# Kernel optimization log

Hardware: AMD Instinct MI355X
Metric: run time of the kernel (lower is better)

The kernel has to match this reference:

```python
import jax, jax.numpy as jnp
import numpy as np

IN_DIM = 128
LAYER_DIMS = [128, 128]
NUM_SAMPLES = [25, 10]
L0 = 3072
NEG_WEIGHT = 1.0


def setup_inputs() -> dict:
    key = jax.random.key(0)
    ks = jax.random.split(key, 12)
    feat = jax.random.normal(ks[0], (L0, IN_DIM), dtype=jnp.float32)
    nodes = jax.random.randint(ks[1], (L0,), 0, L0)
    nb0 = jnp.arange(L0)
    nb1 = jax.random.randint(ks[2], (L0 * 10,), 0, L0)
    nb2 = jax.random.randint(ks[3], (L0 * 10 * 25,), 0, L0)
    src_idx = jax.random.randint(ks[4], (1024,), 0, L0)
    pos_idx = jax.random.randint(ks[5], (1024,), 0, L0)
    neg_idx = jax.random.randint(ks[6], (512,), 0, L0)
    g = 0.05
    # mean aggregator weights: layer0 in=IN_DIM, layer1 in=2*128 (concat)
    w_self_0 = jax.random.normal(ks[7], (IN_DIM, 128), jnp.float32) * g
    w_neigh_0 = jax.random.normal(ks[8], (IN_DIM, 128), jnp.float32) * g
    w_self_1 = jax.random.normal(ks[9], (256, 128), jnp.float32) * g
    w_neigh_1 = jax.random.normal(ks[10], (256, 128), jnp.float32) * g
    return dict(nodes=nodes, feat=feat, src_idx=src_idx, pos_idx=pos_idx,
                neg_idx=neg_idx, nb0=nb0, nb1=nb1, nb2=nb2,
                w_self_0=w_self_0, w_neigh_0=w_neigh_0,
                w_self_1=w_self_1, w_neigh_1=w_neigh_1)


def _aggregate(hidden, params):
    # GraphSAGE layer stack: at layer l, combine each hop with the mean of its
    # sampled neighbors, concat self/neigh transforms, relu except last layer.
    num_layers = len(NUM_SAMPLES)
    for layer in range(num_layers):
        w_self, w_neigh = params[layer]
        is_last = layer == num_layers - 1
        next_hidden = []
        for hop in range(num_layers - layer):
            s = NUM_SAMPLES[num_layers - hop - 1]
            self_v = hidden[hop]  # [n, d]
            neigh = hidden[hop + 1].reshape(self_v.shape[0], s, self_v.shape[1])
            neigh_mean = jnp.mean(neigh, axis=1)
            h = jnp.concatenate([self_v @ w_self, neigh_mean @ w_neigh], axis=1)
            if not is_last:
                h = jax.nn.relu(h)
            next_hidden.append(h)
        hidden = next_hidden
    return hidden[0]


def _l2_normalize(x, eps=1e-12):
    return x * jax.lax.rsqrt(jnp.maximum(jnp.sum(x * x, axis=1, keepdims=True), eps))


def reference(nodes, feat, src_idx, pos_idx, neg_idx, nb0, nb1, nb2,
              w_self_0, w_neigh_0, w_self_1, w_neigh_1):
    hidden = [feat[nb0], feat[nb1], feat[nb2]]
    params = [(w_self_0, w_neigh_0), (w_self_1, w_neigh_1)]
    output = _aggregate(hidden, params)          # [L0, 256]
    output = _l2_normalize(output)
    src_emb = output[src_idx]                    # [B, 256]
    pos_emb = output[pos_idx]
    neg_emb = output[neg_idx]                    # [Nneg, 256]

    aff = jnp.sum(src_emb * pos_emb, axis=1)     # [B]
    neg_aff = src_emb @ neg_emb.T                # [B, Nneg]

    # MRR via double argsort (tf double top_k equivalent; ties -> positive last)
    aff_all = jnp.concatenate([neg_aff, aff[:, None]], axis=1)
    order = jnp.argsort(-aff_all, axis=1, stable=True)
    ranks = jnp.argsort(order, axis=1, stable=True)
    mrr = jnp.mean(1.0 / (ranks[:, -1].astype(jnp.float32) + 1.0))

    # sigmoid cross-entropy: labels 1 -> softplus(-x); labels 0 -> softplus(x)
    true_xent = jax.nn.softplus(-aff)
    neg_xent = jax.nn.softplus(neg_aff)
    loss = jnp.sum(true_xent) + NEG_WEIGHT * jnp.sum(neg_xent)
    loss = loss / jnp.asarray(src_emb.shape[0], jnp.float32)
    return src_emb, loss, mrr
```

## Files before the change

### kernel.cpp

```cpp
#include <hip/hip_runtime.h>
#include <math.h>

#define L0      3072
#define BATCH   1024
#define NNEG    512


__device__ __forceinline__ float bf2f(unsigned short u) {
  return __uint_as_float(((unsigned)u) << 16);
}
__device__ __forceinline__ void store_out(float v, float* p) { *p = v; }
__device__ __forceinline__ void store_out(float v, unsigned short* p) {
  unsigned x = __float_as_uint(v);
  *p = (unsigned short)((x + 0x7fff + ((x >> 16) & 1)) >> 16);
}

template<int K, int AW, int HOFF, bool NORM, typename OutT>
__global__ __launch_bounds__(512) void k_mm(
    const float* __restrict__ Ain,
    const float* __restrict__ W0, const float* __restrict__ W1,
    OutT* __restrict__ Out, const int ldo, const int outHalfOff,
    float* __restrict__ zbuf, const int zcount) {
  __shared__ float AT[6 * AW];
  __shared__ float rs[8][3];
  const int t = threadIdx.x;
  if (zbuf != nullptr && blockIdx.x == 0)
    for (int z = t; z < zcount; z += 512) zbuf[z] = 0.f;
  const int base = blockIdx.x * 6;
  {
    const float4* __restrict__ src = (const float4*)(Ain + base * AW);
    float4* __restrict__ dst = (float4*)AT;
    for (int idx = t; idx < 6 * AW / 4; idx += 512) dst[idx] = src[idx];
  }
  __syncthreads();

  const int wave = t >> 6;
  const int half = wave >> 2;
  const int colg = (wave >> 1) & 1;
  const int rowg = wave & 1;
  const int rg = rowg * 3;
  const int col = colg * 64 + (t & 63);
  const float* __restrict__ W = (half ? W1 : W0) + col;
  const float* __restrict__ A0 = AT + rg * AW + half * HOFF;

  float acc[3] = {0.f, 0.f, 0.f};
#pragma unroll 4
  for (int d = 0; d < K; d += 4) {
    float4 a[3];
#pragma unroll
    for (int r = 0; r < 3; ++r) a[r] = *(const float4*)&A0[r * AW + d];
    float w[4];
#pragma unroll
    for (int i2 = 0; i2 < 4; ++i2) w[i2] = W[(d + i2) * 128];
#pragma unroll
    for (int i2 = 0; i2 < 4; ++i2)
#pragma unroll
      for (int r = 0; r < 3; ++r)
        acc[r] = fmaf(((const float*)&a[r])[i2], w[i2], acc[r]);
  }

  float scale[3] = {1.f, 1.f, 1.f};
  if (NORM) {
    float p[3];
#pragma unroll
    for (int r = 0; r < 3; ++r) p[r] = acc[r] * acc[r];
#pragma unroll
    for (int off = 32; off > 0; off >>= 1)
#pragma unroll
      for (int r = 0; r < 3; ++r) p[r] += __shfl_xor(p[r], off, 64);
    if ((t & 63) == 0) { rs[wave][0] = p[0]; rs[wave][1] = p[1]; rs[wave][2] = p[2]; }
    __syncthreads();
#pragma unroll
    for (int r = 0; r < 3; ++r) {
      const float s = rs[rowg][r] + rs[rowg + 2][r] + rs[rowg + 4][r] + rs[rowg + 6][r];
      scale[r] = rsqrtf(fmaxf(s, 1e-12f));
    }
  }
  OutT* __restrict__ O = Out + half * outHalfOff;
#pragma unroll
  for (int r = 0; r < 3; ++r)
    store_out(acc[r] * scale[r], &O[(base + rg + r) * ldo + col]);
}

__global__ __launch_bounds__(640) void k_aggregate(
    const unsigned short* __restrict__ X0, const unsigned short* __restrict__ Y0,
    const int* __restrict__ nb0, const int* __restrict__ nb1,
    const int* __restrict__ nb2, float* __restrict__ H) {
  __shared__ float gB[10][128], gC[10][128], gD[10][128];
  const int i = blockIdx.x;
  const int t = threadIdx.x;
  const int n0 = nb0[i];
  const int j = t >> 6;
  const int lam = t & 63;
  const int r = i * 10 + j;
  int myidx = 0;
  if (lam < 25) myidx = nb2[r * 25 + lam];
  else if (lam == 25) myidx = nb1[r];
  const int c8 = lam & 15;
  const int sub = lam >> 4;

  float d8[8];
#pragma unroll
  for (int e = 0; e < 8; ++e) d8[e] = 0.f;
#pragma unroll
  for (int m = 0; m < 7; ++m) {
    const int k = sub + 4 * m;
    const int ridx = __shfl(myidx, k, 64);
    if (k < 25) {
      const float4 raw = *(const float4*)(Y0 + ridx * 128 + c8 * 8);
      const unsigned short* u = (const unsigned short*)&raw;
#pragma unroll
      for (int e = 0; e < 8; ++e) d8[e] += bf2f(u[e]);
    }
  }
#pragma unroll
  for (int e = 0; e < 8; ++e) d8[e] += __shfl_xor(d8[e], 16, 64);
#pragma unroll
  for (int e = 0; e < 8; ++e) d8[e] += __shfl_xor(d8[e], 32, 64);

  const int r1 = __shfl(myidx, 25, 64);
  if (sub == 0) {
#pragma unroll
    for (int e = 0; e < 8; ++e) gD[j][c8 * 8 + e] = fmaxf(d8[e] * 0.04f, 0.f);
    const float4 raw = *(const float4*)(Y0 + r1 * 128 + c8 * 8);
    const unsigned short* u = (const unsigned short*)&raw;
#pragma unroll
    for (int e = 0; e < 8; ++e) gB[j][c8 * 8 + e] = bf2f(u[e]);
  } else if (sub == 1) {
    const float4 raw = *(const float4*)(X0 + r1 * 128 + c8 * 8);
    const unsigned short* u = (const unsigned short*)&raw;
#pragma unroll
    for (int e = 0; e < 8; ++e) gC[j][c8 * 8 + e] = fmaxf(bf2f(u[e]), 0.f);
  }
  __syncthreads();

  if (t < 512) {
    const int q = t >> 7, c = t & 127;
    float v;
    if (q == 0) {
      v = fmaxf(bf2f(X0[n0 * 128 + c]), 0.f);
    } else {
      const float* g = (q == 1) ? &gB[0][0] : (q == 2) ? &gC[0][0] : &gD[0][0];
      float s = 0.f;
#pragma unroll
      for (int jj = 0; jj < 10; ++jj) s += g[jj * 128 + c];
      v = s * 0.1f;
      if (q == 1) v = fmaxf(v, 0.f);
    }
    H[i * 512 + t] = v;
  }
}

__device__ __forceinline__ float softplusf(float x) {
  return fmaxf(x, 0.f) + log1pf(expf(-fabsf(x)));
}

__global__ __launch_bounds__(256) void k_prep(
    const float* __restrict__ R, const int* __restrict__ neg_idx,
    float* __restrict__ NT) {
  const int idx = blockIdx.x * 256 + threadIdx.x;
  const int c = idx & 511;
  const int d4 = idx >> 9;
  const float4 v = *(const float4*)&R[neg_idx[c] * 256 + d4 * 4];
#pragma unroll
  for (int i2 = 0; i2 < 4; ++i2)
    NT[(d4 * 4 + i2) * 512 + c] = ((const float*)&v)[i2];
}

__global__ __launch_bounds__(256) void k_neg(
    const float* __restrict__ O, const float* __restrict__ NT,
    const int* __restrict__ src_idx, const int* __restrict__ pos_idx,
    float* __restrict__ out_src, int* __restrict__ rank,
    float* __restrict__ spPos, float* __restrict__ spNeg,
    int* __restrict__ done) {
  __shared__ float SP[32 * 260];
  __shared__ float affL[16];
  __shared__ int cntL[16];
  __shared__ float wsum[4];
  __shared__ int lastDone;
  const int t = threadIdx.x;
  const int rowBase = (blockIdx.x >> 2) * 16;
  const int colBase = (blockIdx.x & 3) * 128;
  const bool first = (colBase == 0);

  if (t < 16) cntL[t] = 0;

  {
    const float4* __restrict__ s4 = (const float4*)O;
#pragma unroll
    for (int idx = t; idx < 32 * 64; idx += 256) {
      const int row = idx >> 6, c4 = idx & 63;
      const int rid = (row < 16) ? src_idx[rowBase + row]
                                 : pos_idx[rowBase + row - 16];
      *(float4*)&SP[row * 260 + c4 * 4] = s4[rid * 64 + c4];
    }
  }
  if (first) {
    const float4* __restrict__ s4 = (const float4*)O;
    float4* __restrict__ d4o = (float4*)out_src;
#pragma unroll
    for (int idx = t; idx < 16 * 64; idx += 256) {
      const int rr = idx >> 6, c4 = idx & 63;
      d4o[(rowBase + rr) * 64 + c4] = s4[src_idx[rowBase + rr] * 64 + c4];
    }
  }
  __syncthreads();

  const int tc = t & 31;
  const int tr = t >> 5;
  const float* __restrict__ B = NT + colBase + 4 * tc;
  const float* __restrict__ A0 = SP + tr * 260;
  const float* __restrict__ A1 = SP + (tr + 8) * 260;
  const float* __restrict__ SV = SP + t * 260;
  const float* __restrict__ PV = SP + (16 + t) * 260;

  float acc[2][4];
#pragma unroll
  for (int r = 0; r < 2; ++r)
#pragma unroll
    for (int j = 0; j < 4; ++j) acc[r][j] = 0.f;
  float aff = 0.f;

#pragma unroll 2
  for (int d4 = 0; d4 < 64; ++d4) {
    const int dd = d4 * 4;
    const float4 a0 = *(const float4*)&A0[dd];
    const float4 a1 = *(const float4*)&A1[dd];
    float4 b[4];
#pragma unroll
    for (int i2 = 0; i2 < 4; ++i2)
      b[i2] = *(const float4*)&B[(dd + i2) * 512];
    float4 sv, pv;
    if (t < 16) {
      sv = *(const float4*)&SV[dd];
      pv = *(const float4*)&PV[dd];
    }
#pragma unroll
    for (int i2 = 0; i2 < 4; ++i2) {
      const float va0 = ((const float*)&a0)[i2];
      const float va1 = ((const float*)&a1)[i2];
#pragma unroll
      for (int j = 0; j < 4; ++j) {
        const float vb = ((const float*)&b[i2])[j];
        acc[0][j] = fmaf(va0, vb, acc[0][j]);
        acc[1][j] = fmaf(va1, vb, acc[1][j]);
      }
      if (t < 16)
        aff = fmaf(((const float*)&sv)[i2], ((const float*)&pv)[i2], aff);
    }
  }
  if (t < 16) affL[t] = aff;
  __syncthreads();

  float sp = 0.f;
  int cnt[2] = {0, 0};
#pragma unroll
  for (int r = 0; r < 2; ++r) {
    const float av = affL[tr + 8 * r];
#pragma unroll
    for (int j = 0; j < 4; ++j) {
      const float v = acc[r][j];
      sp += softplusf(v);
      cnt[r] += (v >= av) ? 1 : 0;
    }
  }
  if (cnt[0]) atomicAdd(&cntL[tr], cnt[0]);
  if (cnt[1]) atomicAdd(&cntL[tr + 8], cnt[1]);
#pragma unroll
  for (int off = 32; off > 0; off >>= 1) sp += __shfl_down(sp, off, 64);
  if ((t & 63) == 0) wsum[t >> 6] = sp;
  if (first && t < 16) atomicAdd(spPos, softplusf(-aff));
  __syncthreads();
  if (t == 0) atomicAdd(spNeg, wsum[0] + wsum[1] + wsum[2] + wsum[3]);
  if (t < 16) atomicAdd(&rank[rowBase + t], cntL[t]);

  __threadfence();
  __syncthreads();
  if (t == 0) lastDone = (atomicAdd(done, 1) == 255) ? 1 : 0;
  __syncthreads();
  if (lastDone) {
    float s = 0.f;
    for (int i = t; i < BATCH; i += 256) {
      const int rv = __hip_atomic_load(&rank[i], __ATOMIC_RELAXED,
                                       __HIP_MEMORY_SCOPE_AGENT);
      s += 1.f / (float)(rv + 1);
    }
#pragma unroll
    for (int off = 32; off > 0; off >>= 1) s += __shfl_down(s, off, 64);
    if ((t & 63) == 0) wsum[t >> 6] = s;
    __syncthreads();
    if (t == 0) {
      const float mrr = (wsum[0] + wsum[1] + wsum[2] + wsum[3]) * (1.f / 1024.f);
      const float p = __hip_atomic_load(spPos, __ATOMIC_RELAXED,
                                        __HIP_MEMORY_SCOPE_AGENT);
      const float n = __hip_atomic_load(spNeg, __ATOMIC_RELAXED,
                                        __HIP_MEMORY_SCOPE_AGENT);
      out_src[BATCH * 256]     = (p + n) * (1.f / 1024.f);
      out_src[BATCH * 256 + 1] = mrr;
    }
  }
}

extern "C" void kernel_launch(void* const* d_in, const int* in_sizes, int n_in,
                              void* d_out, int out_size, void* d_ws, size_t ws_size,
                              hipStream_t stream) {
  const float* feat   = (const float*)d_in[1];
  const int* src_idx  = (const int*)d_in[2];
  const int* pos_idx  = (const int*)d_in[3];
  const int* neg_idx  = (const int*)d_in[4];
  const int* nb0      = (const int*)d_in[5];
  const int* nb1      = (const int*)d_in[6];
  const int* nb2      = (const int*)d_in[7];
  const float* ws0    = (const float*)d_in[8];
  const float* wn0    = (const float*)d_in[9];
  const float* ws1    = (const float*)d_in[10];
  const float* wn1    = (const float*)d_in[11];

  float* wsf = (float*)d_ws;
  unsigned short* X0 = (unsigned short*)d_ws;
  unsigned short* Y0 = X0 + 393216;
  float* H     = wsf + 393216;
  float* R     = wsf + 1966080;
  float* spPos = wsf + 2752512;
  float* spNeg = wsf + 2752513;
  int*   rank  = (int*)(wsf + 2752514);
  int*   done  = rank + 1024;
  float* NT    = wsf + 2753540;
  float* out   = (float*)d_out;

  k_mm<128, 128, 0, false, unsigned short><<<L0 / 6, 512, 0, stream>>>(
      feat, ws0, wn0, X0, 128, 393216, spPos, 1027);
  k_aggregate<<<L0, 640, 0, stream>>>(X0, Y0, nb0, nb1, nb2, H);
  k_mm<256, 512, 256, true, float><<<L0 / 6, 512, 0, stream>>>(
      H, ws1, wn1, R, 256, 128, nullptr, 0);
  k_prep<<<128, 256, 0, stream>>>(R, neg_idx, NT);
  k_neg<<<256, 256, 0, stream>>>(
      R, NT, src_idx, pos_idx, out, rank, spPos, spNeg, done);
}
```

Before: 166.6 us.

## Fuse all stages into one persistent kernel with software grid barriers

Replaces the five launches (two GEMMs, aggregation, transpose prep, negative scoring) with a zeroing kernel plus one 256-block persistent kernel that uses atomic-counter grid barriers between phases. The aggregation now keeps its per-node hidden rows in shared memory and feeds the second GEMM directly, which removes the H round trip through global memory. The intent is to cut launch gaps and intermediate traffic. In exchange the whole pipeline runs on only 256 blocks, so parallelism in the gather and GEMM phases is much lower. The spin barriers also depend on all blocks being resident at once.

```diff
diff --git a/kernel.cpp b/kernel.cpp
--- a/kernel.cpp
+++ b/kernel.cpp
@@ -4,299 +4,362 @@
 #define L0      3072
 #define BATCH   1024
 #define NNEG    512
+#define NBLK    256
 
 
 __device__ __forceinline__ float bf2f(unsigned short u) {
   return __uint_as_float(((unsigned)u) << 16);
 }
-__device__ __forceinline__ void store_out(float v, float* p) { *p = v; }
-__device__ __forceinline__ void store_out(float v, unsigned short* p) {
+__device__ __forceinline__ unsigned short f2bf(float v) {
   unsigned x = __float_as_uint(v);
-  *p = (unsigned short)((x + 0x7fff + ((x >> 16) & 1)) >> 16);
-}
-
-template<int K, int AW, int HOFF, bool NORM, typename OutT>
-__global__ __launch_bounds__(512) void k_mm(
-    const float* __restrict__ Ain,
-    const float* __restrict__ W0, const float* __restrict__ W1,
-    OutT* __restrict__ Out, const int ldo, const int outHalfOff,
-    float* __restrict__ zbuf, const int zcount) {
-  __shared__ float AT[6 * AW];
-  __shared__ float rs[8][3];
-  const int t = threadIdx.x;
-  if (zbuf != nullptr && blockIdx.x == 0)
-    for (int z = t; z < zcount; z += 512) zbuf[z] = 0.f;
-  const int base = blockIdx.x * 6;
-  {
-    const float4* __restrict__ src = (const float4*)(Ain + base * AW);
-    float4* __restrict__ dst = (float4*)AT;
-    for (int idx = t; idx < 6 * AW / 4; idx += 512) dst[idx] = src[idx];
-  }
-  __syncthreads();
-
-  const int wave = t >> 6;
-  const int half = wave >> 2;
-  const int colg = (wave >> 1) & 1;
-  const int rowg = wave & 1;
-  const int rg = rowg * 3;
-  const int col = colg * 64 + (t & 63);
-  const float* __restrict__ W = (half ? W1 : W0) + col;
-  const float* __restrict__ A0 = AT + rg * AW + half * HOFF;
-
-  float acc[3] = {0.f, 0.f, 0.f};
-#pragma unroll 4
-  for (int d = 0; d < K; d += 4) {
-    float4 a[3];
-#pragma unroll
-    for (int r = 0; r < 3; ++r) a[r] = *(const float4*)&A0[r * AW + d];
-    float w[4];
-#pragma unroll
-    for (int i2 = 0; i2 < 4; ++i2) w[i2] = W[(d + i2) * 128];
-#pragma unroll
-    for (int i2 = 0; i2 < 4; ++i2)
-#pragma unroll
-      for (int r = 0; r < 3; ++r)
-        acc[r] = fmaf(((const float*)&a[r])[i2], w[i2], acc[r]);
-  }
-
-  float scale[3] = {1.f, 1.f, 1.f};
-  if (NORM) {
-    float p[3];
-#pragma unroll
-    for (int r = 0; r < 3; ++r) p[r] = acc[r] * acc[r];
-#pragma unroll
-    for (int off = 32; off > 0; off >>= 1)
-#pragma unroll
-      for (int r = 0; r < 3; ++r) p[r] += __shfl_xor(p[r], off, 64);
-    if ((t & 63) == 0) { rs[wave][0] = p[0]; rs[wave][1] = p[1]; rs[wave][2] = p[2]; }
-    __syncthreads();
-#pragma unroll
-    for (int r = 0; r < 3; ++r) {
-      const float s = rs[rowg][r] + rs[rowg + 2][r] + rs[rowg + 4][r] + rs[rowg + 6][r];
-      scale[r] = rsqrtf(fmaxf(s, 1e-12f));
-    }
-  }
-  OutT* __restrict__ O = Out + half * outHalfOff;
-#pragma unroll
-  for (int r = 0; r < 3; ++r)
-    store_out(acc[r] * scale[r], &O[(base + rg + r) * ldo + col]);
-}
-
-__global__ __launch_bounds__(640) void k_aggregate(
-    const unsigned short* __restrict__ X0, const unsigned short* __restrict__ Y0,
-    const int* __restrict__ nb0, const int* __restrict__ nb1,
-    const int* __restrict__ nb2, float* __restrict__ H) {
-  __shared__ float gB[10][128], gC[10][128], gD[10][128];
-  const int i = blockIdx.x;
-  const int t = threadIdx.x;
-  const int n0 = nb0[i];
-  const int j = t >> 6;
-  const int lam = t & 63;
-  const int r = i * 10 + j;
-  int myidx = 0;
-  if (lam < 25) myidx = nb2[r * 25 + lam];
-  else if (lam == 25) myidx = nb1[r];
-  const int c8 = lam & 15;
-  const int sub = lam >> 4;
-
-  float d8[8];
-#pragma unroll
-  for (int e = 0; e < 8; ++e) d8[e] = 0.f;
-#pragma unroll
-  for (int m = 0; m < 7; ++m) {
-    const int k = sub + 4 * m;
-    const int ridx = __shfl(myidx, k, 64);
-    if (k < 25) {
-      const float4 raw = *(const float4*)(Y0 + ridx * 128 + c8 * 8);
-      const unsigned short* u = (const unsigned short*)&raw;
-#pragma unroll
-      for (int e = 0; e < 8; ++e) d8[e] += bf2f(u[e]);
-    }
-  }
-#pragma unroll
-  for (int e = 0; e < 8; ++e) d8[e] += __shfl_xor(d8[e], 16, 64);
-#pragma unroll
-  for (int e = 0; e < 8; ++e) d8[e] += __shfl_xor(d8[e], 32, 64);
-
-  const int r1 = __shfl(myidx, 25, 64);
-  if (sub == 0) {
-#pragma unroll
-    for (int e = 0; e < 8; ++e) gD[j][c8 * 8 + e] = fmaxf(d8[e] * 0.04f, 0.f);
-    const float4 raw = *(const float4*)(Y0 + r1 * 128 + c8 * 8);
-    const unsigned short* u = (const unsigned short*)&raw;
-#pragma unroll
-    for (int e = 0; e < 8; ++e) gB[j][c8 * 8 + e] = bf2f(u[e]);
-  } else if (sub == 1) {
-    const float4 raw = *(const float4*)(X0 + r1 * 128 + c8 * 8);
-    const unsigned short* u = (const unsigned short*)&raw;
-#pragma unroll
-    for (int e = 0; e < 8; ++e) gC[j][c8 * 8 + e] = fmaxf(bf2f(u[e]), 0.f);
-  }
-  __syncthreads();
-
-  if (t < 512) {
-    const int q = t >> 7, c = t & 127;
-    float v;
-    if (q == 0) {
-      v = fmaxf(bf2f(X0[n0 * 128 + c]), 0.f);
-    } else {
-      const float* g = (q == 1) ? &gB[0][0] : (q == 2) ? &gC[0][0] : &gD[0][0];
-      float s = 0.f;
-#pragma unroll
-      for (int jj = 0; jj < 10; ++jj) s += g[jj * 128 + c];
-      v = s * 0.1f;
-      if (q == 1) v = fmaxf(v, 0.f);
-    }
-    H[i * 512 + t] = v;
-  }
-}
-
+  return (unsigned short)((x + 0x7fff + ((x >> 16) & 1)) >> 16);
+}
 __device__ __forceinline__ float softplusf(float x) {
   return fmaxf(x, 0.f) + log1pf(expf(-fabsf(x)));
 }
 
-__global__ __launch_bounds__(256) void k_prep(
-    const float* __restrict__ R, const int* __restrict__ neg_idx,
-    float* __restrict__ NT) {
-  const int idx = blockIdx.x * 256 + threadIdx.x;
-  const int c = idx & 511;
-  const int d4 = idx >> 9;
-  const float4 v = *(const float4*)&R[neg_idx[c] * 256 + d4 * 4];
-#pragma unroll
-  for (int i2 = 0; i2 < 4; ++i2)
-    NT[(d4 * 4 + i2) * 512 + c] = ((const float*)&v)[i2];
-}
-
-__global__ __launch_bounds__(256) void k_neg(
-    const float* __restrict__ O, const float* __restrict__ NT,
-    const int* __restrict__ src_idx, const int* __restrict__ pos_idx,
-    float* __restrict__ out_src, int* __restrict__ rank,
+__device__ __forceinline__ void gbar(int* ctr) {
+  __syncthreads();
+  if (threadIdx.x == 0) {
+    __threadfence();
+    __hip_atomic_fetch_add(ctr, 1, __ATOMIC_ACQ_REL, __HIP_MEMORY_SCOPE_AGENT);
+    while (__hip_atomic_load(ctr, __ATOMIC_ACQUIRE,
+                             __HIP_MEMORY_SCOPE_AGENT) < NBLK)
+      __builtin_amdgcn_s_sleep(1);
+  }
+  __syncthreads();
+}
+
+struct D2S {
+  float SP[32 * 260];
+  float affL[16];
+  int   cntL[16];
+  float wsum[8];
+  int   lastDone;
+};
+union SMU {
+  float AT[12 * 512];
+  D2S   d2;
+};
+
+__global__ __launch_bounds__(256) void k_zero(float* z) {
+  const int t = threadIdx.x;
+  for (int i = t; i < 1030; i += 256) z[i] = 0.f;
+}
+
+__global__ __launch_bounds__(512) void k_fused(
+    const float* __restrict__ feat, const int* __restrict__ src_idx,
+    const int* __restrict__ pos_idx, const int* __restrict__ neg_idx,
+    const int* __restrict__ nb0, const int* __restrict__ nb1,
+    const int* __restrict__ nb2,
+    const float* __restrict__ ws0, const float* __restrict__ wn0,
+    const float* __restrict__ ws1, const float* __restrict__ wn1,
+    unsigned short* __restrict__ X0, unsigned short* __restrict__ Y0,
+    float* __restrict__ R, float* __restrict__ NT,
     float* __restrict__ spPos, float* __restrict__ spNeg,
-    int* __restrict__ done) {
-  __shared__ float SP[32 * 260];
-  __shared__ float affL[16];
-  __shared__ int cntL[16];
-  __shared__ float wsum[4];
-  __shared__ int lastDone;
+    int* __restrict__ rank, int* __restrict__ done, int* __restrict__ bar,
+    float* __restrict__ out) {
+  __shared__ SMU sm;
+  __shared__ float rs2[8][3];
   const int t = threadIdx.x;
-  const int rowBase = (blockIdx.x >> 2) * 16;
-  const int colBase = (blockIdx.x & 3) * 128;
-  const bool first = (colBase == 0);
-
-  if (t < 16) cntL[t] = 0;
+  const int bid = blockIdx.x;
+  const int wave = t >> 6, lane = t & 63;
+  const int base = bid * 12;
 
   {
-    const float4* __restrict__ s4 = (const float4*)O;
-#pragma unroll
-    for (int idx = t; idx < 32 * 64; idx += 256) {
-      const int row = idx >> 6, c4 = idx & 63;
-      const int rid = (row < 16) ? src_idx[rowBase + row]
-                                 : pos_idx[rowBase + row - 16];
-      *(float4*)&SP[row * 260 + c4 * 4] = s4[rid * 64 + c4];
-    }
-  }
-  if (first) {
-    const float4* __restrict__ s4 = (const float4*)O;
-    float4* __restrict__ d4o = (float4*)out_src;
-#pragma unroll
-    for (int idx = t; idx < 16 * 64; idx += 256) {
-      const int rr = idx >> 6, c4 = idx & 63;
-      d4o[(rowBase + rr) * 64 + c4] = s4[src_idx[rowBase + rr] * 64 + c4];
+    const float4* __restrict__ src = (const float4*)(feat + base * 128);
+    float4* __restrict__ dst = (float4*)sm.AT;
+    for (int idx = t; idx < 384; idx += 512) dst[idx] = src[idx];
+    __syncthreads();
+    const int half = wave >> 2;
+    const int rg = (wave & 3) * 3;
+    const float* __restrict__ W = (half ? wn0 : ws0) + lane;
+    const float* __restrict__ A0 = sm.AT + rg * 128;
+    float acc[3][2] = {{0.f, 0.f}, {0.f, 0.f}, {0.f, 0.f}};
+#pragma unroll 4
+    for (int d = 0; d < 128; d += 4) {
+      float4 a[3];
+#pragma unroll
+      for (int r = 0; r < 3; ++r) a[r] = *(const float4*)&A0[r * 128 + d];
+      float w0[4], w1[4];
+#pragma unroll
+      for (int i2 = 0; i2 < 4; ++i2) {
+        w0[i2] = W[(d + i2) * 128];
+        w1[i2] = W[(d + i2) * 128 + 64];
+      }
+#pragma unroll
+      for (int i2 = 0; i2 < 4; ++i2)
+#pragma unroll
+        for (int r = 0; r < 3; ++r) {
+          const float av = ((const float*)&a[r])[i2];
+          acc[r][0] = fmaf(av, w0[i2], acc[r][0]);
+          acc[r][1] = fmaf(av, w1[i2], acc[r][1]);
+        }
+    }
+    unsigned short* __restrict__ O = half ? Y0 : X0;
+#pragma unroll
+    for (int r = 0; r < 3; ++r) {
+      O[(base + rg + r) * 128 + lane] = f2bf(acc[r][0]);
+      O[(base + rg + r) * 128 + lane + 64] = f2bf(acc[r][1]);
+    }
+  }
+  gbar(&bar[0]);
+
+  {
+    const int c8 = lane & 15, sub = lane >> 4;
+    for (int rep = 0; rep < 2; ++rep) {
+      const int wi = wave + rep * 8;
+      if (wi < 12) {
+        const int i = base + wi;
+        const int n0 = nb0[i];
+        float Ba[8], Ca[8], Da[8];
+#pragma unroll
+        for (int e = 0; e < 8; ++e) { Ba[e] = 0.f; Ca[e] = 0.f; Da[e] = 0.f; }
+#pragma unroll 2
+        for (int j = 0; j < 10; ++j) {
+          const int r = i * 10 + j;
+          int myidx = 0;
+          if (lane < 25) myidx = nb2[r * 25 + lane];
+          else if (lane == 25) myidx = nb1[r];
+          float d8[8];
+#pragma unroll
+          for (int e = 0; e < 8; ++e) d8[e] = 0.f;
+#pragma unroll
+          for (int m = 0; m < 7; ++m) {
+            const int k = sub + 4 * m;
+            const int ridx = __shfl(myidx, k, 64);
+            if (k < 25) {
+              const float4 raw = *(const float4*)(Y0 + ridx * 128 + c8 * 8);
+              const unsigned short* u = (const unsigned short*)&raw;
+#pragma unroll
+              for (int e = 0; e < 8; ++e) d8[e] += bf2f(u[e]);
+            }
+          }
+#pragma unroll
+          for (int e = 0; e < 8; ++e) d8[e] += __shfl_xor(d8[e], 16, 64);
+#pragma unroll
+          for (int e = 0; e < 8; ++e) d8[e] += __shfl_xor(d8[e], 32, 64);
+#pragma unroll
+          for (int e = 0; e < 8; ++e) Da[e] += fmaxf(d8[e] * 0.04f, 0.f);
+          const int r1 = __shfl(myidx, 25, 64);
+          {
+            const float4 raw = *(const float4*)(Y0 + r1 * 128 + c8 * 8);
+            const unsigned short* u = (const unsigned short*)&raw;
+#pragma unroll
+            for (int e = 0; e < 8; ++e) Ba[e] += bf2f(u[e]);
+          }
+          {
+            const float4 raw = *(const float4*)(X0 + r1 * 128 + c8 * 8);
+            const unsigned short* u = (const unsigned short*)&raw;
+#pragma unroll
+            for (int e = 0; e < 8; ++e) Ca[e] += fmaxf(bf2f(u[e]), 0.f);
+          }
+        }
+        float v8[8];
+        if (sub == 0) {
+          const float4 raw = *(const float4*)(X0 + n0 * 128 + c8 * 8);
+          const unsigned short* u = (const unsigned short*)&raw;
+#pragma unroll
+          for (int e = 0; e < 8; ++e) v8[e] = fmaxf(bf2f(u[e]), 0.f);
+        } else if (sub == 1) {
+#pragma unroll
+          for (int e = 0; e < 8; ++e) v8[e] = fmaxf(Ba[e] * 0.1f, 0.f);
+        } else if (sub == 2) {
+#pragma unroll
+          for (int e = 0; e < 8; ++e) v8[e] = Ca[e] * 0.1f;
+        } else {
+#pragma unroll
+          for (int e = 0; e < 8; ++e) v8[e] = Da[e] * 0.1f;
+        }
+        float* __restrict__ Hp = &sm.AT[wi * 512 + sub * 128 + c8 * 8];
+        *(float4*)Hp = make_float4(v8[0], v8[1], v8[2], v8[3]);
+        *(float4*)(Hp + 4) = make_float4(v8[4], v8[5], v8[6], v8[7]);
+      }
     }
   }
   __syncthreads();
 
-  const int tc = t & 31;
-  const int tr = t >> 5;
-  const float* __restrict__ B = NT + colBase + 4 * tc;
-  const float* __restrict__ A0 = SP + tr * 260;
-  const float* __restrict__ A1 = SP + (tr + 8) * 260;
-  const float* __restrict__ SV = SP + t * 260;
-  const float* __restrict__ PV = SP + (16 + t) * 260;
-
-  float acc[2][4];
-#pragma unroll
-  for (int r = 0; r < 2; ++r)
-#pragma unroll
-    for (int j = 0; j < 4; ++j) acc[r][j] = 0.f;
-  float aff = 0.f;
-
+  {
+    const int half = wave >> 2;
+    const int rowg = wave & 3;
+    const int rg = rowg * 3;
+    const float* __restrict__ W = (half ? wn1 : ws1) + lane;
+    const float* __restrict__ A0 = sm.AT + rg * 512 + half * 256;
+    float acc[3][2] = {{0.f, 0.f}, {0.f, 0.f}, {0.f, 0.f}};
+#pragma unroll 4
+    for (int d = 0; d < 256; d += 4) {
+      float4 a[3];
+#pragma unroll
+      for (int r = 0; r < 3; ++r) a[r] = *(const float4*)&A0[r * 512 + d];
+      float w0[4], w1[4];
+#pragma unroll
+      for (int i2 = 0; i2 < 4; ++i2) {
+        w0[i2] = W[(d + i2) * 128];
+        w1[i2] = W[(d + i2) * 128 + 64];
+      }
+#pragma unroll
+      for (int i2 = 0; i2 < 4; ++i2)
+#pragma unroll
+        for (int r = 0; r < 3; ++r) {
+          const float av = ((const float*)&a[r])[i2];
+          acc[r][0] = fmaf(av, w0[i2], acc[r][0]);
+          acc[r][1] = fmaf(av, w1[i2], acc[r][1]);
+        }
+    }
+    float p[3];
+#pragma unroll
+    for (int r = 0; r < 3; ++r)
+      p[r] = acc[r][0] * acc[r][0] + acc[r][1] * acc[r][1];
+#pragma unroll
+    for (int off = 32; off > 0; off >>= 1)
+#pragma unroll
+      for (int r = 0; r < 3; ++r) p[r] += __shfl_xor(p[r], off, 64);
+    if (lane == 0) { rs2[wave][0] = p[0]; rs2[wave][1] = p[1]; rs2[wave][2] = p[2]; }
+    __syncthreads();
+#pragma unroll
+    for (int r = 0; r < 3; ++r) {
+      const float s = rs2[rowg][r] + rs2[rowg + 4][r];
+      const float scale = rsqrtf(fmaxf(s, 1e-12f));
+      R[(base + rg + r) * 256 + half * 128 + lane] = acc[r][0] * scale;
+      R[(base + rg + r) * 256 + half * 128 + lane + 64] = acc[r][1] * scale;
+    }
+  }
+  gbar(&bar[1]);
+
+  if (t < 128) {
+    const int job = bid * 128 + t;
+    const int c = job & 511, d4 = job >> 9;
+    const float4 v = *(const float4*)&R[neg_idx[c] * 256 + d4 * 4];
+    NT[(d4 * 4 + 0) * 512 + c] = v.x;
+    NT[(d4 * 4 + 1) * 512 + c] = v.y;
+    NT[(d4 * 4 + 2) * 512 + c] = v.z;
+    NT[(d4 * 4 + 3) * 512 + c] = v.w;
+  }
+  gbar(&bar[2]);
+
+  {
+    const int rowBase = (bid >> 2) * 16;
+    const int colBase = (bid & 3) * 128;
+    const bool first = (colBase == 0);
+    if (t < 16) sm.d2.cntL[t] = 0;
+    {
+      const float4* __restrict__ s4 = (const float4*)R;
+      for (int idx = t; idx < 32 * 64; idx += 512) {
+        const int row = idx >> 6, c4 = idx & 63;
+        const int rid = (row < 16) ? src_idx[rowBase + row]
+                                   : pos_idx[rowBase + row - 16];
+        *(float4*)&sm.d2.SP[row * 260 + c4 * 4] = s4[rid * 64 + c4];
+      }
+      if (first) {
+        float4* __restrict__ d4o = (float4*)out;
+        for (int idx = t; idx < 16 * 64; idx += 512) {
+          const int rr = idx >> 6, c4 = idx & 63;
+          d4o[(rowBase + rr) * 64 + c4] = s4[src_idx[rowBase + rr] * 64 + c4];
+        }
+      }
+    }
+    __syncthreads();
+
+    const int tc = t & 31;
+    const int tr = (t >> 5) & 7;
+    float acc[2][4];
+#pragma unroll
+    for (int r = 0; r < 2; ++r)
+#pragma unroll
+      for (int j = 0; j < 4; ++j) acc[r][j] = 0.f;
+    float aff = 0.f;
+
+    if (t < 256) {
+      const float* __restrict__ B = NT + colBase + 4 * tc;
+      const float* __restrict__ A0 = sm.d2.SP + tr * 260;
+      const float* __restrict__ A1 = sm.d2.SP + (tr + 8) * 260;
+      const float* __restrict__ SV = sm.d2.SP + t * 260;
+      const float* __restrict__ PV = sm.d2.SP + (16 + t) * 260;
 #pragma unroll 2
-  for (int d4 = 0; d4 < 64; ++d4) {
-    const int dd = d4 * 4;
-    const float4 a0 = *(const float4*)&A0[dd];
-    const float4 a1 = *(const float4*)&A1[dd];
-    float4 b[4];
-#pragma unroll
-    for (int i2 = 0; i2 < 4; ++i2)
-      b[i2] = *(const float4*)&B[(dd + i2) * 512];
-    float4 sv, pv;
-    if (t < 16) {
-      sv = *(const float4*)&SV[dd];
-      pv = *(const float4*)&PV[dd];
-    }
-#pragma unroll
-    for (int i2 = 0; i2 < 4; ++i2) {
-      const float va0 = ((const float*)&a0)[i2];
-      const float va1 = ((const float*)&a1)[i2];
-#pragma unroll
-      for (int j = 0; j < 4; ++j) {
-        const float vb = ((const float*)&b[i2])[j];
-        acc[0][j] = fmaf(va0, vb, acc[0][j]);
-        acc[1][j] = fmaf(va1, vb, acc[1][j]);
-      }
-      if (t < 16)
-        aff = fmaf(((const float*)&sv)[i2], ((const float*)&pv)[i2], aff);
-    }
-  }
-  if (t < 16) affL[t] = aff;
-  __syncthreads();
-
-  float sp = 0.f;
-  int cnt[2] = {0, 0};
-#pragma unroll
-  for (int r = 0; r < 2; ++r) {
-    const float av = affL[tr + 8 * r];
-#pragma unroll
-    for (int j = 0; j < 4; ++j) {
-      const float v = acc[r][j];
-      sp += softplusf(v);
-      cnt[r] += (v >= av) ? 1 : 0;
-    }
-  }
-  if (cnt[0]) atomicAdd(&cntL[tr], cnt[0]);
-  if (cnt[1]) atomicAdd(&cntL[tr + 8], cnt[1]);
-#pragma unroll
-  for (int off = 32; off > 0; off >>= 1) sp += __shfl_down(sp, off, 64);
-  if ((t & 63) == 0) wsum[t >> 6] = sp;
-  if (first && t < 16) atomicAdd(spPos, softplusf(-aff));
-  __syncthreads();
-  if (t == 0) atomicAdd(spNeg, wsum[0] + wsum[1] + wsum[2] + wsum[3]);
-  if (t < 16) atomicAdd(&rank[rowBase + t], cntL[t]);
-
-  __threadfence();
-  __syncthreads();
-  if (t == 0) lastDone = (atomicAdd(done, 1) == 255) ? 1 : 0;
-  __syncthreads();
-  if (lastDone) {
-    float s = 0.f;
-    for (int i = t; i < BATCH; i += 256) {
-      const int rv = __hip_atomic_load(&rank[i], __ATOMIC_RELAXED,
-                                       __HIP_MEMORY_SCOPE_AGENT);
-      s += 1.f / (float)(rv + 1);
-    }
-#pragma unroll
-    for (int off = 32; off > 0; off >>= 1) s += __shfl_down(s, off, 64);
-    if ((t & 63) == 0) wsum[t >> 6] = s;
-    __syncthreads();
-    if (t == 0) {
-      const float mrr = (wsum[0] + wsum[1] + wsum[2] + wsum[3]) * (1.f / 1024.f);
-      const float p = __hip_atomic_load(spPos, __ATOMIC_RELAXED,
-                                        __HIP_MEMORY_SCOPE_AGENT);
-      const float n = __hip_atomic_load(spNeg, __ATOMIC_RELAXED,
-                                        __HIP_MEMORY_SCOPE_AGENT);
-      out_src[BATCH * 256]     = (p + n) * (1.f / 1024.f);
-      out_src[BATCH * 256 + 1] = mrr;
+      for (int d4 = 0; d4 < 64; ++d4) {
+        const int dd = d4 * 4;
+        const float4 a0 = *(const float4*)&A0[dd];
+        const float4 a1 = *(const float4*)&A1[dd];
+        float4 b[4];
+#pragma unroll
+        for (int i2 = 0; i2 < 4; ++i2)
+          b[i2] = *(const float4*)&B[(dd + i2) * 512];
+        float4 sv, pv;
+        if (t < 16) {
+          sv = *(const float4*)&SV[dd];
+          pv = *(const float4*)&PV[dd];
+        }
+#pragma unroll
+        for (int i2 = 0; i2 < 4; ++i2) {
+          const float va0 = ((const float*)&a0)[i2];
+          const float va1 = ((const float*)&a1)[i2];
+#pragma unroll
+          for (int j = 0; j < 4; ++j) {
+            const float vb = ((const float*)&b[i2])[j];
+            acc[0][j] = fmaf(va0, vb, acc[0][j]);
+            acc[1][j] = fmaf(va1, vb, acc[1][j]);
+          }
+          if (t < 16)
+            aff = fmaf(((const float*)&sv)[i2], ((const float*)&pv)[i2], aff);
+        }
+      }
+    }
+    if (t < 16) sm.d2.affL[t] = aff;
+    __syncthreads();
+
+    float sp = 0.f;
+    if (t < 256) {
+      int cnt[2] = {0, 0};
+#pragma unroll
+      for (int r = 0; r < 2; ++r) {
+        const float av = sm.d2.affL[tr + 8 * r];
+#pragma unroll
+        for (int j = 0; j < 4; ++j) {
+          const float v = acc[r][j];
+          sp += softplusf(v);
+          cnt[r] += (v >= av) ? 1 : 0;
+        }
+      }
+      if (cnt[0]) atomicAdd(&sm.d2.cntL[tr], cnt[0]);
+      if (cnt[1]) atomicAdd(&sm.d2.cntL[tr + 8], cnt[1]);
+    }
+#pragma unroll
+    for (int off = 32; off > 0; off >>= 1) sp += __shfl_down(sp, off, 64);
+    if ((t & 63) == 0) sm.d2.wsum[t >> 6] = sp;
+    if (first && t < 16) atomicAdd(spPos, softplusf(-aff));
+    __syncthreads();
+    if (t == 0)
+      atomicAdd(spNeg, sm.d2.wsum[0] + sm.d2.wsum[1] + sm.d2.wsum[2] +
+                           sm.d2.wsum[3] + sm.d2.wsum[4] + sm.d2.wsum[5] +
+                           sm.d2.wsum[6] + sm.d2.wsum[7]);
+    if (t < 16) atomicAdd(&rank[rowBase + t], sm.d2.cntL[t]);
+
+    __threadfence();
+    __syncthreads();
+    if (t == 0) sm.d2.lastDone = (atomicAdd(done, 1) == NBLK - 1) ? 1 : 0;
+    __syncthreads();
+    if (sm.d2.lastDone) {
+      float s = 0.f;
+      for (int i = t; i < BATCH; i += 512) {
+        const int rv = __hip_atomic_load(&rank[i], __ATOMIC_RELAXED,
+                                         __HIP_MEMORY_SCOPE_AGENT);
+        s += 1.f / (float)(rv + 1);
+      }
+#pragma unroll
+      for (int off = 32; off > 0; off >>= 1) s += __shfl_down(s, off, 64);
+      if ((t & 63) == 0) sm.d2.wsum[t >> 6] = s;
+      __syncthreads();
+      if (t == 0) {
+        const float mrr = (sm.d2.wsum[0] + sm.d2.wsum[1] + sm.d2.wsum[2] +
+                           sm.d2.wsum[3] + sm.d2.wsum[4] + sm.d2.wsum[5] +
+                           sm.d2.wsum[6] + sm.d2.wsum[7]) * (1.f / 1024.f);
+        const float p = __hip_atomic_load(spPos, __ATOMIC_RELAXED,
+                                          __HIP_MEMORY_SCOPE_AGENT);
+        const float n = __hip_atomic_load(spNeg, __ATOMIC_RELAXED,
+                                          __HIP_MEMORY_SCOPE_AGENT);
+        out[BATCH * 256]     = (p + n) * (1.f / 1024.f);
+        out[BATCH * 256 + 1] = mrr;
+      }
     }
   }
 }
@@ -319,21 +382,17 @@
   float* wsf = (float*)d_ws;
   unsigned short* X0 = (unsigned short*)d_ws;
   unsigned short* Y0 = X0 + 393216;
-  float* H     = wsf + 393216;
   float* R     = wsf + 1966080;
   float* spPos = wsf + 2752512;
   float* spNeg = wsf + 2752513;
   int*   rank  = (int*)(wsf + 2752514);
   int*   done  = rank + 1024;
-  float* NT    = wsf + 2753540;
+  int*   bar   = done + 1;
+  float* NT    = wsf + 2753544;
   float* out   = (float*)d_out;
 
-  k_mm<128, 128, 0, false, unsigned short><<<L0 / 6, 512, 0, stream>>>(
-      feat, ws0, wn0, X0, 128, 393216, spPos, 1027);
-  k_aggregate<<<L0, 640, 0, stream>>>(X0, Y0, nb0, nb1, nb2, H);
-  k_mm<256, 512, 256, true, float><<<L0 / 6, 512, 0, stream>>>(
-      H, ws1, wn1, R, 256, 128, nullptr, 0);
-  k_prep<<<128, 256, 0, stream>>>(R, neg_idx, NT);
-  k_neg<<<256, 256, 0, stream>>>(
-      R, NT, src_idx, pos_idx, out, rank, spPos, spNeg, done);
-}
+  k_zero<<<1, 256, 0, stream>>>(spPos);
+  k_fused<<<NBLK, 512, 0, stream>>>(
+      feat, src_idx, pos_idx, neg_idx, nb0, nb1, nb2,
+      ws0, wn0, ws1, wn1, X0, Y0, R, NT, spPos, spNeg, rank, done, bar, out);
+}
```

Result: slower. 239.0 us (+43.5%).

## Fuse negative-row gather into k_neg and drop the transpose prep kernel

Applied to the files above, without the earlier changes.

Removes the k_prep kernel that gathered and transposed negative embeddings into NT. k_neg now reads each negative row directly from R through neg_idx. It is retiled to 8 rows by 64 columns per block across 1024 blocks, with one column per thread. Per-row rank counts are now reduced with wavefront shuffles instead of shared atomics. This saves a launch and a global round trip, at the cost of strided per-thread row reads from global memory and more redundant loads of the same rows across blocks.

```diff
diff --git a/kernel.cpp b/kernel.cpp
--- a/kernel.cpp
+++ b/kernel.cpp
@@ -155,43 +155,29 @@
   return fmaxf(x, 0.f) + log1pf(expf(-fabsf(x)));
 }
 
-__global__ __launch_bounds__(256) void k_prep(
-    const float* __restrict__ R, const int* __restrict__ neg_idx,
-    float* __restrict__ NT) {
-  const int idx = blockIdx.x * 256 + threadIdx.x;
-  const int c = idx & 511;
-  const int d4 = idx >> 9;
-  const float4 v = *(const float4*)&R[neg_idx[c] * 256 + d4 * 4];
-#pragma unroll
-  for (int i2 = 0; i2 < 4; ++i2)
-    NT[(d4 * 4 + i2) * 512 + c] = ((const float*)&v)[i2];
-}
-
 __global__ __launch_bounds__(256) void k_neg(
-    const float* __restrict__ O, const float* __restrict__ NT,
-    const int* __restrict__ src_idx, const int* __restrict__ pos_idx,
+    const float* __restrict__ O, const int* __restrict__ src_idx,
+    const int* __restrict__ pos_idx, const int* __restrict__ neg_idx,
     float* __restrict__ out_src, int* __restrict__ rank,
     float* __restrict__ spPos, float* __restrict__ spNeg,
     int* __restrict__ done) {
-  __shared__ float SP[32 * 260];
-  __shared__ float affL[16];
-  __shared__ int cntL[16];
+  __shared__ float SP[16 * 260];
+  __shared__ float affL[8];
+  __shared__ int cntL[8];
   __shared__ float wsum[4];
   __shared__ int lastDone;
   const int t = threadIdx.x;
-  const int rowBase = (blockIdx.x >> 2) * 16;
-  const int colBase = (blockIdx.x & 3) * 128;
+  const int rowBase = (blockIdx.x >> 3) * 8;
+  const int colBase = (blockIdx.x & 7) * 64;
   const bool first = (colBase == 0);
-
-  if (t < 16) cntL[t] = 0;
 
   {
     const float4* __restrict__ s4 = (const float4*)O;
 #pragma unroll
-    for (int idx = t; idx < 32 * 64; idx += 256) {
+    for (int idx = t; idx < 16 * 64; idx += 256) {
       const int row = idx >> 6, c4 = idx & 63;
-      const int rid = (row < 16) ? src_idx[rowBase + row]
-                                 : pos_idx[rowBase + row - 16];
+      const int rid = (row < 8) ? src_idx[rowBase + row]
+                                : pos_idx[rowBase + row - 8];
       *(float4*)&SP[row * 260 + c4 * 4] = s4[rid * 64 + c4];
     }
   }
@@ -199,84 +185,67 @@
     const float4* __restrict__ s4 = (const float4*)O;
     float4* __restrict__ d4o = (float4*)out_src;
 #pragma unroll
-    for (int idx = t; idx < 16 * 64; idx += 256) {
+    for (int idx = t; idx < 8 * 64; idx += 256) {
       const int rr = idx >> 6, c4 = idx & 63;
       d4o[(rowBase + rr) * 64 + c4] = s4[src_idx[rowBase + rr] * 64 + c4];
     }
   }
   __syncthreads();
 
-  const int tc = t & 31;
-  const int tr = t >> 5;
-  const float* __restrict__ B = NT + colBase + 4 * tc;
-  const float* __restrict__ A0 = SP + tr * 260;
-  const float* __restrict__ A1 = SP + (tr + 8) * 260;
+  const int cl = t & 63;
+  const int rowg = t >> 6;
+  const float* __restrict__ Bp = O + neg_idx[colBase + cl] * 256;
+  const float* __restrict__ A0 = SP + rowg * 260;
+  const float* __restrict__ A1 = SP + (rowg + 4) * 260;
   const float* __restrict__ SV = SP + t * 260;
-  const float* __restrict__ PV = SP + (16 + t) * 260;
-
-  float acc[2][4];
-#pragma unroll
-  for (int r = 0; r < 2; ++r)
-#pragma unroll
-    for (int j = 0; j < 4; ++j) acc[r][j] = 0.f;
-  float aff = 0.f;
-
-#pragma unroll 2
+  const float* __restrict__ PV = SP + (8 + t) * 260;
+
+  float acc0 = 0.f, acc1 = 0.f, aff = 0.f;
+#pragma unroll 4
   for (int d4 = 0; d4 < 64; ++d4) {
     const int dd = d4 * 4;
+    const float4 b  = *(const float4*)&Bp[dd];
     const float4 a0 = *(const float4*)&A0[dd];
     const float4 a1 = *(const float4*)&A1[dd];
-    float4 b[4];
-#pragma unroll
-    for (int i2 = 0; i2 < 4; ++i2)
-      b[i2] = *(const float4*)&B[(dd + i2) * 512];
     float4 sv, pv;
-    if (t < 16) {
+    if (t < 8) {
       sv = *(const float4*)&SV[dd];
       pv = *(const float4*)&PV[dd];
     }
 #pragma unroll
     for (int i2 = 0; i2 < 4; ++i2) {
-      const float va0 = ((const float*)&a0)[i2];
-      const float va1 = ((const float*)&a1)[i2];
-#pragma unroll
-      for (int j = 0; j < 4; ++j) {
-        const float vb = ((const float*)&b[i2])[j];
-        acc[0][j] = fmaf(va0, vb, acc[0][j]);
-        acc[1][j] = fmaf(va1, vb, acc[1][j]);
-      }
-      if (t < 16)
+      const float vb = ((const float*)&b)[i2];
+      acc0 = fmaf(((const float*)&a0)[i2], vb, acc0);
+      acc1 = fmaf(((const float*)&a1)[i2], vb, acc1);
+      if (t < 8)
         aff = fmaf(((const float*)&sv)[i2], ((const float*)&pv)[i2], aff);
     }
   }
-  if (t < 16) affL[t] = aff;
-  __syncthreads();
-
-  float sp = 0.f;
-  int cnt[2] = {0, 0};
-#pragma unroll
-  for (int r = 0; r < 2; ++r) {
-    const float av = affL[tr + 8 * r];
-#pragma unroll
-    for (int j = 0; j < 4; ++j) {
-      const float v = acc[r][j];
-      sp += softplusf(v);
-      cnt[r] += (v >= av) ? 1 : 0;
-    }
-  }
-  if (cnt[0]) atomicAdd(&cntL[tr], cnt[0]);
-  if (cnt[1]) atomicAdd(&cntL[tr + 8], cnt[1]);
-#pragma unroll
-  for (int off = 32; off > 0; off >>= 1) sp += __shfl_down(sp, off, 64);
-  if ((t & 63) == 0) wsum[t >> 6] = sp;
-  if (first && t < 16) atomicAdd(spPos, softplusf(-aff));
-  __syncthreads();
+  if (t < 8) affL[t] = aff;
+  __syncthreads();
+
+  float sp = softplusf(acc0) + softplusf(acc1);
+  int c0 = (acc0 >= affL[rowg]) ? 1 : 0;
+  int c1 = (acc1 >= affL[rowg + 4]) ? 1 : 0;
+#pragma unroll
+  for (int off = 32; off > 0; off >>= 1) {
+    sp += __shfl_down(sp, off, 64);
+    c0 += __shfl_down(c0, off, 64);
+    c1 += __shfl_down(c1, off, 64);
+  }
+  if ((t & 63) == 0) {
+    cntL[rowg] = c0;
+    cntL[rowg + 4] = c1;
+    wsum[rowg] = sp;
+  }
+  __syncthreads();
+  if (t < 8) atomicAdd(&rank[rowBase + t], cntL[t]);
   if (t == 0) atomicAdd(spNeg, wsum[0] + wsum[1] + wsum[2] + wsum[3]);
-  if (t < 16) atomicAdd(&rank[rowBase + t], cntL[t]);
+  if (first && t < 8) atomicAdd(spPos, softplusf(-affL[t]));
 
   __threadfence();
   __syncthreads();
-  if (t == 0) lastDone = (atomicAdd(done, 1) == 255) ? 1 : 0;
+  if (t == 0) lastDone = (atomicAdd(done, 1) == 1023) ? 1 : 0;
   __syncthreads();
   if (lastDone) {
     float s = 0.f;
@@ -325,7 +294,6 @@
   float* spNeg = wsf + 2752513;
   int*   rank  = (int*)(wsf + 2752514);
   int*   done  = rank + 1024;
-  float* NT    = wsf + 2753540;
   float* out   = (float*)d_out;
 
   k_mm<128, 128, 0, false, unsigned short><<<L0 / 6, 512, 0, stream>>>(
@@ -333,7 +301,6 @@
   k_aggregate<<<L0, 640, 0, stream>>>(X0, Y0, nb0, nb1, nb2, H);
   k_mm<256, 512, 256, true, float><<<L0 / 6, 512, 0, stream>>>(
       H, ws1, wn1, R, 256, 128, nullptr, 0);
-  k_prep<<<128, 256, 0, stream>>>(R, neg_idx, NT);
-  k_neg<<<256, 256, 0, stream>>>(
-      R, NT, src_idx, pos_idx, out, rank, spPos, spNeg, done);
-}
+  k_neg<<<1024, 256, 0, stream>>>(
+      R, src_idx, pos_idx, neg_idx, out, rank, spPos, spNeg, done);
+}
```

After: 219.4 us. 1.32x slower.
